# Optimization experiments

Measured on AMD Instinct MI355X. Metric: run time of the kernel, lower is better.

Reference implementation:

```python
import jax, jax.numpy as jnp
import numpy as np

B, N, DIM = 2, 2048, 1024
HEADS, DIM_HEAD, ROT = 16, 64, 32
SCALE = DIM_HEAD ** -0.5
INNER = HEADS * DIM_HEAD


def rotate_half(x):
    # '... (j d) -> ... j d' with j=2 -> split into first/second half
    d = x.shape[-1] // 2
    x1, x2 = x[..., :d], x[..., d:]
    return jnp.concatenate([-x2, x1], axis=-1)


def apply_rotary_pos_emb(freqs, t):
    rot = freqs.shape[-1]
    t1, t_pass = t[..., :rot], t[..., rot:]
    t1 = t1 * jnp.cos(freqs) + rotate_half(t1) * jnp.sin(freqs)
    return jnp.concatenate([t1, t_pass], axis=-1)


def setup_inputs() -> dict:
    key = jax.random.key(0)
    ks = jax.random.split(key, 5)
    x = jax.random.normal(ks[0], (B, N, DIM), dtype=jnp.float32)
    mask = jnp.ones((B, N), dtype=bool)
    rotary_pos_emb = jax.random.normal(ks[1], (N, ROT), dtype=jnp.float32)
    w_qkv = jax.random.normal(ks[2], (DIM, 3 * INNER), dtype=jnp.float32) * (DIM ** -0.5)
    w_out = jax.random.normal(ks[3], (INNER, DIM), dtype=jnp.float32) * (INNER ** -0.5)
    g = jnp.ones((DIM,), dtype=jnp.float32)
    return {"x": x, "mask": mask, "rotary_pos_emb": rotary_pos_emb,
            "w_qkv": w_qkv, "w_out": w_out, "g": g}


def reference(x, mask, rotary_pos_emb, w_qkv, w_out, g):
    b, n, _ = x.shape
    qkv = x @ w_qkv  # [b, n, 3*inner]
    q, k, v = jnp.split(qkv, 3, axis=-1)
    def to_heads(t):
        return t.reshape(b, n, HEADS, DIM_HEAD).transpose(0, 2, 1, 3)  # b h n d
    q, k, v = to_heads(q), to_heads(k), to_heads(v)
    q = q * SCALE
    # note: original applies rotary to q, k AND v
    q = apply_rotary_pos_emb(rotary_pos_emb, q)
    k = apply_rotary_pos_emb(rotary_pos_emb, k)
    v = apply_rotary_pos_emb(rotary_pos_emb, v)
    sim = jnp.einsum('bhid,bhjd->bhij', q, k)  # [b, h, n, n]
    neg = -jnp.finfo(sim.dtype).max
    sim = jnp.where(mask[:, None, None, :], sim, neg)
    causal_mask = jnp.triu(jnp.ones((n, n), dtype=bool), 1)
    sim = jnp.where(causal_mask, neg, sim)
    attn = jax.nn.softmax(sim.astype(jnp.float32), axis=-1).astype(sim.dtype)
    out = jnp.einsum('bhij,bhjd->bhid', attn, v)
    out = out.transpose(0, 2, 1, 3).reshape(b, n, INNER)
    out = out @ w_out
    # LayerNorm (no bias), eps=1e-5 for fp32, biased variance
    mean = jnp.mean(out, axis=-1, keepdims=True)
    var = jnp.var(out, axis=-1, keepdims=True)
    return (out - mean) * jax.lax.rsqrt(var + 1e-5) * g
```

## Files before the change

kernel.cpp:

```cpp
#include <hip/hip_runtime.h>
#include <stdint.h>

typedef unsigned short u16;
typedef __bf16 bf16x8 __attribute__((ext_vector_type(8)));
typedef float f32x4 __attribute__((ext_vector_type(4)));

#define B_ 2
#define N_ 2048
#define H_ 16
#define SCALE_ 0.125f
#define FM_ 11.0f

__device__ __forceinline__ float b2f(u16 u) {
    unsigned v = (unsigned)u << 16;
    float f;
    __builtin_memcpy(&f, &v, 4);
    return f;
}
__device__ __forceinline__ u16 f2b(float f) {
    unsigned x;
    __builtin_memcpy(&x, &f, 4);
    x = x + 0x7fff + ((x >> 16) & 1);
    return (u16)(x >> 16);
}

__global__ __launch_bounds__(256) void sentinel(float* __restrict__ out, int n, float val) {
    int i = blockIdx.x * 256 + threadIdx.x;
    if (i < n) out[i] = val;
}

__global__ __launch_bounds__(256) void conv_f2b(const float* __restrict__ in,
                                                u16* __restrict__ out, int n) {
    int i = (blockIdx.x * 256 + threadIdx.x) * 4;
    if (i >= n) return;
    float4 v = *(const float4*)(in + i);
    ushort4 o;
    o.x = f2b(v.x); o.y = f2b(v.y); o.z = f2b(v.z); o.w = f2b(v.w);
    *(ushort4*)(out + i) = o;
}

__global__ __launch_bounds__(256) void transpose_f2b(const float* __restrict__ in,
                                                     u16* __restrict__ out, int R, int C) {
    __shared__ float tile[32][33];
    int tx = threadIdx.x, ty = threadIdx.y;
    int c0 = blockIdx.x * 32, r0 = blockIdx.y * 32;
#pragma unroll
    for (int i = 0; i < 32; i += 8) tile[ty + i][tx] = in[(size_t)(r0 + ty + i) * C + c0 + tx];
    __syncthreads();
#pragma unroll
    for (int i = 0; i < 32; i += 8) out[(size_t)(c0 + ty + i) * R + r0 + tx] = f2b(tile[tx][ty + i]);
}

__global__ __launch_bounds__(256) void gemm_qkv(const u16* __restrict__ A, const u16* __restrict__ Bt,
                                                const float* __restrict__ freqs,
                                                u16* __restrict__ qo, u16* __restrict__ ko,
                                                u16* __restrict__ vt) {
    __shared__ __align__(16) u16 As[64 * 40];
    __shared__ __align__(16) u16 Bs[64 * 40];
    const int tid = threadIdx.x;
    const int wave = tid >> 6, lane = tid & 63;
    const int l15 = lane & 15, q4 = lane >> 4;
    const int m0 = blockIdx.y * 64, n0 = blockIdx.x * 64;
    const int srow = tid >> 2, scol = (tid & 3) * 8;
    f32x4 acc[4];
#pragma unroll
    for (int i = 0; i < 4; i++) acc[i] = (f32x4){0.f, 0.f, 0.f, 0.f};
    for (int k0 = 0; k0 < 1024; k0 += 32) {
        *(uint4*)&As[srow * 40 + scol] = *(const uint4*)&A[(size_t)(m0 + srow) * 1024 + k0 + scol];
        *(uint4*)&Bs[srow * 40 + scol] = *(const uint4*)&Bt[(size_t)(n0 + srow) * 1024 + k0 + scol];
        __syncthreads();
        bf16x8 a = *(const bf16x8*)&As[(wave * 16 + l15) * 40 + q4 * 8];
#pragma unroll
        for (int nt = 0; nt < 4; nt++) {
            bf16x8 b = *(const bf16x8*)&Bs[(nt * 16 + l15) * 40 + q4 * 8];
            acc[nt] = __builtin_amdgcn_mfma_f32_16x16x32_bf16(a, b, acc[nt], 0, 0, 0);
        }
        __syncthreads();
    }
    const int t = n0 >> 10;
    const int h = (n0 & 1023) >> 6;
#pragma unroll
    for (int r = 0; r < 4; r++) {
        int gm = m0 + wave * 16 + q4 * 4 + r;
        int b = gm >> 11, n = gm & 2047;
        float x0 = acc[0][r], x1 = acc[1][r], x2 = acc[2][r], x3 = acc[3][r];
        float f1 = freqs[n * 32 + l15];
        float f2 = freqs[n * 32 + 16 + l15];
        if (t == 0) { x0 *= SCALE_; x1 *= SCALE_; x2 *= SCALE_; x3 *= SCALE_; }
        float r0 = x0 * cosf(f1) - x1 * sinf(f1);
        float r1 = x1 * cosf(f2) + x0 * sinf(f2);
        int bh = b * H_ + h;
        if (t == 2) {
            u16* o = vt + (size_t)bh * 64 * N_;
            o[(l15) * N_ + n] = f2b(r0);
            o[(l15 + 16) * N_ + n] = f2b(r1);
            o[(l15 + 32) * N_ + n] = f2b(x2);
            o[(l15 + 48) * N_ + n] = f2b(x3);
        } else {
            u16* dst = (t == 0) ? qo : ko;
            u16* p = dst + ((size_t)bh * N_ + n) * 64;
            p[l15] = f2b(r0);
            p[l15 + 16] = f2b(r1);
            p[l15 + 32] = f2b(x2);
            p[l15 + 48] = f2b(x3);
        }
    }
}

__global__ __launch_bounds__(256) void attn(const u16* __restrict__ q, const u16* __restrict__ k,
                                            const u16* __restrict__ vt, u16* __restrict__ out) {
    __shared__ __align__(16) u16 Ks[2][64 * 72];
    __shared__ __align__(16) u16 Vs[2][64 * 72];
    __shared__ __align__(16) u16 Ps[64 * 72];
    const int tid = threadIdx.x, wave = tid >> 6, lane = tid & 63;
    const int l15 = lane & 15, q4 = lane >> 4;
    const int ta = blockIdx.x, tb = 31 - ta, bh = blockIdx.y;
    const u16* qp = q + (size_t)bh * N_ * 64;
    const u16* kp = k + (size_t)bh * N_ * 64;
    const u16* vp = vt + (size_t)bh * 64 * N_;
    const int b = bh >> 4, h = bh & 15;
    const int srow8 = tid >> 3, scol8 = (tid & 7) * 8;
    const int prow = (wave * 16 + l15) * 72;

    bf16x8 aqA0, aqA1, aqB0, aqB1;
    {
        int qr = ta * 64 + wave * 16;
        aqA0 = *(const bf16x8*)&qp[(qr + l15) * 64 + q4 * 8];
        aqA1 = *(const bf16x8*)&qp[(qr + l15) * 64 + 32 + q4 * 8];
        qr = tb * 64 + wave * 16;
        aqB0 = *(const bf16x8*)&qp[(qr + l15) * 64 + q4 * 8];
        aqB1 = *(const bf16x8*)&qp[(qr + l15) * 64 + 32 + q4 * 8];
    }
    f32x4 o[4];
#pragma unroll
    for (int i = 0; i < 4; i++) o[i] = (f32x4){0.f, 0.f, 0.f, 0.f};
    float psum = 0.f;

    auto stage = [&](int jt, int buf) {
#pragma unroll
        for (int i = 0; i < 64; i += 32) {
            *(uint4*)&Ks[buf][(i + srow8) * 72 + scol8] =
                *(const uint4*)&kp[(size_t)(jt * 64 + i + srow8) * 64 + scol8];
            *(uint4*)&Vs[buf][(i + srow8) * 72 + scol8] =
                *(const uint4*)&vp[(size_t)(i + srow8) * N_ + jt * 64 + scol8];
        }
    };
    auto iter = [&](bf16x8 aq0, bf16x8 aq1, int cur, int domask, int qa, int jb) {
#pragma unroll
        for (int kt = 0; kt < 4; kt++) {
            bf16x8 kf0 = *(const bf16x8*)&Ks[cur][(kt * 16 + l15) * 72 + q4 * 8];
            bf16x8 kf1 = *(const bf16x8*)&Ks[cur][(kt * 16 + l15) * 72 + 32 + q4 * 8];
            f32x4 z = (f32x4){0.f, 0.f, 0.f, 0.f};
            z = __builtin_amdgcn_mfma_f32_16x16x32_bf16(kf0, aq0, z, 0, 0, 0);
            z = __builtin_amdgcn_mfma_f32_16x16x32_bf16(kf1, aq1, z, 0, 0, 0);
            union { u16 u[4]; uint2 v; } pk;
            float ps = 0.f;
#pragma unroll
            for (int r = 0; r < 4; r++) {
                float s = z[r];
                if (domask) {
                    int key = jb * 64 + kt * 16 + q4 * 4 + r;
                    if (key > qa) s = -1e30f;
                }
                float p = __expf(s - FM_);
                ps += p;
                pk.u[r] = f2b(p);
            }
            psum += ps;
            *(uint2*)&Ps[prow + kt * 16 + q4 * 4] = pk.v;
        }
        bf16x8 pf0 = *(const bf16x8*)&Ps[prow + q4 * 8];
        bf16x8 pf1 = *(const bf16x8*)&Ps[prow + 32 + q4 * 8];
#pragma unroll
        for (int dt = 0; dt < 4; dt++) {
            bf16x8 v0 = *(const bf16x8*)&Vs[cur][(dt * 16 + l15) * 72 + q4 * 8];
            bf16x8 v1 = *(const bf16x8*)&Vs[cur][(dt * 16 + l15) * 72 + 32 + q4 * 8];
            o[dt] = __builtin_amdgcn_mfma_f32_16x16x32_bf16(v0, pf0, o[dt], 0, 0, 0);
            o[dt] = __builtin_amdgcn_mfma_f32_16x16x32_bf16(v1, pf1, o[dt], 0, 0, 0);
        }
    };
    auto epilogue = [&](int qt) {
        float v = psum;
        v += __shfl_xor(v, 16);
        v += __shfl_xor(v, 32);
        float inv = 1.f / v;
        int n = qt * 64 + wave * 16 + l15;
        u16* op = out + ((size_t)b * N_ + n) * 1024 + h * 64;
#pragma unroll
        for (int dt = 0; dt < 4; dt++) {
            union { u16 u[4]; uint2 v2; } w;
#pragma unroll
            for (int r = 0; r < 4; r++) w.u[r] = f2b(o[dt][r] * inv);
            *(uint2*)(op + dt * 16 + q4 * 4) = w.v2;
        }
#pragma unroll
        for (int i = 0; i < 4; i++) o[i] = (f32x4){0.f, 0.f, 0.f, 0.f};
        psum = 0.f;
    };

    stage(0, 0);
    int m = 0;
    for (int jb = 0; jb <= ta; jb++, m++) {
        int cur = m & 1;
        __syncthreads();
        stage((jb < ta) ? (jb + 1) : 0, cur ^ 1);
        iter(aqA0, aqA1, cur, jb == ta, ta * 64 + wave * 16 + l15, jb);
    }
    epilogue(ta);
    for (int jb = 0; jb <= tb; jb++, m++) {
        int cur = m & 1;
        __syncthreads();
        if (jb < tb) stage(jb + 1, cur ^ 1);
        iter(aqB0, aqB1, cur, jb == tb, tb * 64 + wave * 16 + l15, jb);
    }
    epilogue(tb);
}

__global__ __launch_bounds__(256) void gemm_out(const u16* __restrict__ A, const u16* __restrict__ Bt,
                                                float* __restrict__ C) {
    __shared__ __align__(16) u16 As[64 * 40];
    __shared__ __align__(16) u16 Bs[64 * 40];
    const int tid = threadIdx.x;
    const int wave = tid >> 6, lane = tid & 63;
    const int l15 = lane & 15, q4 = lane >> 4;
    const int m0 = blockIdx.y * 64, n0 = blockIdx.x * 64;
    const int srow = tid >> 2, scol = (tid & 3) * 8;
    f32x4 acc[4];
#pragma unroll
    for (int i = 0; i < 4; i++) acc[i] = (f32x4){0.f, 0.f, 0.f, 0.f};
    for (int k0 = 0; k0 < 1024; k0 += 32) {
        *(uint4*)&As[srow * 40 + scol] = *(const uint4*)&A[(size_t)(m0 + srow) * 1024 + k0 + scol];
        *(uint4*)&Bs[srow * 40 + scol] = *(const uint4*)&Bt[(size_t)(n0 + srow) * 1024 + k0 + scol];
        __syncthreads();
        bf16x8 a = *(const bf16x8*)&As[(wave * 16 + l15) * 40 + q4 * 8];
#pragma unroll
        for (int nt = 0; nt < 4; nt++) {
            bf16x8 b = *(const bf16x8*)&Bs[(nt * 16 + l15) * 40 + q4 * 8];
            acc[nt] = __builtin_amdgcn_mfma_f32_16x16x32_bf16(a, b, acc[nt], 0, 0, 0);
        }
        __syncthreads();
    }
#pragma unroll
    for (int nt = 0; nt < 4; nt++) {
#pragma unroll
        for (int r = 0; r < 4; r++) {
            int gm = m0 + wave * 16 + q4 * 4 + r;
            int gn = n0 + nt * 16 + l15;
            C[(size_t)gm * 1024 + gn] = acc[nt][r];
        }
    }
}

__global__ __launch_bounds__(256) void lnorm(const float* __restrict__ x, const float* __restrict__ g,
                                             float* __restrict__ out) {
    __shared__ float sh[8];
    int row = blockIdx.x, tid = threadIdx.x;
    float4 v = *(const float4*)(x + (size_t)row * 1024 + tid * 4);
    float s = v.x + v.y + v.z + v.w;
    float sq = v.x * v.x + v.y * v.y + v.z * v.z + v.w * v.w;
#pragma unroll
    for (int m = 1; m < 64; m <<= 1) {
        s += __shfl_xor(s, m);
        sq += __shfl_xor(sq, m);
    }
    if ((tid & 63) == 0) {
        sh[tid >> 6] = s;
        sh[4 + (tid >> 6)] = sq;
    }
    __syncthreads();
    s = sh[0] + sh[1] + sh[2] + sh[3];
    sq = sh[4] + sh[5] + sh[6] + sh[7];
    float mean = s * (1.f / 1024.f);
    float var = fmaxf(sq * (1.f / 1024.f) - mean * mean, 0.f);
    float rstd = rsqrtf(var + 1e-5f);
    float4 gv = *(const float4*)(g + tid * 4);
    float4 ov;
    ov.x = (v.x - mean) * rstd * gv.x;
    ov.y = (v.y - mean) * rstd * gv.y;
    ov.z = (v.z - mean) * rstd * gv.z;
    ov.w = (v.w - mean) * rstd * gv.w;
    *(float4*)(out + (size_t)row * 1024 + tid * 4) = ov;
}

extern "C" void kernel_launch(void* const* d_in, const int* in_sizes, int n_in,
                              void* d_out, int out_size, void* d_ws, size_t ws_size,
                              hipStream_t stream) {
    const float* x = nullptr;
    const float* rotf = nullptr;
    const float* wqkv = nullptr;
    const float* wout = nullptr;
    const float* g = nullptr;
    for (int i = 0; i < n_in; i++) {
        switch (in_sizes[i]) {
            case 4194304: x = (const float*)d_in[i]; break;
            case 65536:   rotf = (const float*)d_in[i]; break;
            case 3145728: wqkv = (const float*)d_in[i]; break;
            case 1048576: wout = (const float*)d_in[i]; break;
            case 1024:    g = (const float*)d_in[i]; break;
            default: break;
        }
    }
    int oblk = (out_size + 255) / 256;
    if (!(x && rotf && wqkv && wout && g)) {
        sentinel<<<oblk, 256, 0, stream>>>((float*)d_out, out_size, 200.f);
        return;
    }
    const size_t MB = 1024u * 1024;
    if (ws_size < 80 * MB) {
        sentinel<<<oblk, 256, 0, stream>>>((float*)d_out, out_size, 100.f);
        return;
    }
    char* ws = (char*)d_ws;
    u16* wqkvT = (u16*)(ws);
    u16* woutT = (u16*)(ws + 6 * MB);
    u16* xbf = (u16*)(ws + 8 * MB);
    u16* qbuf = (u16*)(ws + 16 * MB);
    u16* kbuf = (u16*)(ws + 24 * MB);
    u16* vtbuf = (u16*)(ws + 32 * MB);
    u16* abuf = (u16*)(ws + 40 * MB);
    float* pbuf = (float*)(ws + 48 * MB);

    conv_f2b<<<4096, 256, 0, stream>>>(x, xbf, 4194304);
    transpose_f2b<<<dim3(96, 32), dim3(32, 8), 0, stream>>>(wqkv, wqkvT, 1024, 3072);
    transpose_f2b<<<dim3(32, 32), dim3(32, 8), 0, stream>>>(wout, woutT, 1024, 1024);
    gemm_qkv<<<dim3(48, 64), 256, 0, stream>>>(xbf, wqkvT, rotf, qbuf, kbuf, vtbuf);
    attn<<<dim3(16, 32), 256, 0, stream>>>(qbuf, kbuf, vtbuf, abuf);
    gemm_out<<<dim3(16, 64), 256, 0, stream>>>(abuf, woutT, pbuf);
    lnorm<<<4096, 256, 0, stream>>>(pbuf, g, (float*)d_out);
}
```

Before: 240.0 us.

## Enlarge GEMM tiles to 128x128 and stage operands via direct global-to-LDS loads

Both projection GEMMs move from 64x64 block tiles, where each wave did a 16x64 slice, to 128x128 tiles where each wave computes a 64x64 sub-tile with 16 MFMA accumulators. This raises operand reuse from LDS and cuts global traffic per FLOP. Operands are now staged with global_load_lds 16-byte loads straight into unpadded LDS, skipping the register round trip. In exchange the kernels use more registers and launch fewer blocks, and the unpadded LDS layout may cause bank conflicts on fragment reads.

```diff
diff --git a/kernel.cpp b/kernel.cpp
--- a/kernel.cpp
+++ b/kernel.cpp
@@ -22,6 +22,12 @@
     __builtin_memcpy(&x, &f, 4);
     x = x + 0x7fff + ((x >> 16) & 1);
     return (u16)(x >> 16);
+}
+
+typedef const __attribute__((address_space(1))) unsigned int ga_uint;
+typedef __attribute__((address_space(3))) unsigned int ls_uint;
+__device__ __forceinline__ void gld_lds16(const void* g, void* l) {
+    __builtin_amdgcn_global_load_lds((ga_uint*)g, (ls_uint*)l, 16, 0, 0);
 }
 
 __global__ __launch_bounds__(256) void sentinel(float* __restrict__ out, int n, float val) {
@@ -55,54 +61,73 @@
                                                 const float* __restrict__ freqs,
                                                 u16* __restrict__ qo, u16* __restrict__ ko,
                                                 u16* __restrict__ vt) {
-    __shared__ __align__(16) u16 As[64 * 40];
-    __shared__ __align__(16) u16 Bs[64 * 40];
+    __shared__ __align__(16) u16 As[128 * 32];
+    __shared__ __align__(16) u16 Bs[128 * 32];
     const int tid = threadIdx.x;
     const int wave = tid >> 6, lane = tid & 63;
     const int l15 = lane & 15, q4 = lane >> 4;
-    const int m0 = blockIdx.y * 64, n0 = blockIdx.x * 64;
-    const int srow = tid >> 2, scol = (tid & 3) * 8;
-    f32x4 acc[4];
-#pragma unroll
-    for (int i = 0; i < 4; i++) acc[i] = (f32x4){0.f, 0.f, 0.f, 0.f};
+    const int m0 = blockIdx.y * 128, n0 = blockIdx.x * 128;
+    const int wm = (wave & 1) * 64, wn = (wave >> 1) * 64;
+    const int lrow = lane >> 2, lchunk = (lane & 3) * 8;
+    f32x4 acc[4][4];
+#pragma unroll
+    for (int i = 0; i < 4; i++)
+#pragma unroll
+        for (int j = 0; j < 4; j++) acc[i][j] = (f32x4){0.f, 0.f, 0.f, 0.f};
+
     for (int k0 = 0; k0 < 1024; k0 += 32) {
-        *(uint4*)&As[srow * 40 + scol] = *(const uint4*)&A[(size_t)(m0 + srow) * 1024 + k0 + scol];
-        *(uint4*)&Bs[srow * 40 + scol] = *(const uint4*)&Bt[(size_t)(n0 + srow) * 1024 + k0 + scol];
-        __syncthreads();
-        bf16x8 a = *(const bf16x8*)&As[(wave * 16 + l15) * 40 + q4 * 8];
-#pragma unroll
-        for (int nt = 0; nt < 4; nt++) {
-            bf16x8 b = *(const bf16x8*)&Bs[(nt * 16 + l15) * 40 + q4 * 8];
-            acc[nt] = __builtin_amdgcn_mfma_f32_16x16x32_bf16(a, b, acc[nt], 0, 0, 0);
-        }
-        __syncthreads();
-    }
-    const int t = n0 >> 10;
-    const int h = (n0 & 1023) >> 6;
-#pragma unroll
-    for (int r = 0; r < 4; r++) {
-        int gm = m0 + wave * 16 + q4 * 4 + r;
-        int b = gm >> 11, n = gm & 2047;
-        float x0 = acc[0][r], x1 = acc[1][r], x2 = acc[2][r], x3 = acc[3][r];
-        float f1 = freqs[n * 32 + l15];
-        float f2 = freqs[n * 32 + 16 + l15];
-        if (t == 0) { x0 *= SCALE_; x1 *= SCALE_; x2 *= SCALE_; x3 *= SCALE_; }
-        float r0 = x0 * cosf(f1) - x1 * sinf(f1);
-        float r1 = x1 * cosf(f2) + x0 * sinf(f2);
-        int bh = b * H_ + h;
-        if (t == 2) {
-            u16* o = vt + (size_t)bh * 64 * N_;
-            o[(l15) * N_ + n] = f2b(r0);
-            o[(l15 + 16) * N_ + n] = f2b(r1);
-            o[(l15 + 32) * N_ + n] = f2b(x2);
-            o[(l15 + 48) * N_ + n] = f2b(x3);
-        } else {
-            u16* dst = (t == 0) ? qo : ko;
-            u16* p = dst + ((size_t)bh * N_ + n) * 64;
-            p[l15] = f2b(r0);
-            p[l15 + 16] = f2b(r1);
-            p[l15 + 32] = f2b(x2);
-            p[l15 + 48] = f2b(x3);
+#pragma unroll
+        for (int i = 0; i < 2; i++) {
+            int row = wave * 32 + i * 16;
+            gld_lds16(&A[(size_t)(m0 + row + lrow) * 1024 + k0 + lchunk], &As[row * 32]);
+            gld_lds16(&Bt[(size_t)(n0 + row + lrow) * 1024 + k0 + lchunk], &Bs[row * 32]);
+        }
+        __syncthreads();
+        bf16x8 af[4], bf[4];
+#pragma unroll
+        for (int mt = 0; mt < 4; mt++)
+            af[mt] = *(const bf16x8*)&As[(wm + mt * 16 + l15) * 32 + q4 * 8];
+#pragma unroll
+        for (int nt = 0; nt < 4; nt++)
+            bf[nt] = *(const bf16x8*)&Bs[(wn + nt * 16 + l15) * 32 + q4 * 8];
+#pragma unroll
+        for (int mt = 0; mt < 4; mt++)
+#pragma unroll
+            for (int nt = 0; nt < 4; nt++)
+                acc[mt][nt] = __builtin_amdgcn_mfma_f32_16x16x32_bf16(af[mt], bf[nt], acc[mt][nt], 0, 0, 0);
+        __syncthreads();
+    }
+    const int qh = n0 + wn;
+    const int t = qh >> 10;
+    const int h = (qh & 1023) >> 6;
+#pragma unroll
+    for (int mt = 0; mt < 4; mt++) {
+#pragma unroll
+        for (int r = 0; r < 4; r++) {
+            int gm = m0 + wm + mt * 16 + q4 * 4 + r;
+            int b = gm >> 11, n = gm & 2047;
+            float x0 = acc[mt][0][r], x1 = acc[mt][1][r];
+            float x2 = acc[mt][2][r], x3 = acc[mt][3][r];
+            float f1 = freqs[n * 32 + l15];
+            float f2 = freqs[n * 32 + 16 + l15];
+            if (t == 0) { x0 *= SCALE_; x1 *= SCALE_; x2 *= SCALE_; x3 *= SCALE_; }
+            float r0 = x0 * cosf(f1) - x1 * sinf(f1);
+            float r1 = x1 * cosf(f2) + x0 * sinf(f2);
+            int bh = b * H_ + h;
+            if (t == 2) {
+                u16* o = vt + (size_t)bh * 64 * N_;
+                o[(l15) * N_ + n] = f2b(r0);
+                o[(l15 + 16) * N_ + n] = f2b(r1);
+                o[(l15 + 32) * N_ + n] = f2b(x2);
+                o[(l15 + 48) * N_ + n] = f2b(x3);
+            } else {
+                u16* dst = (t == 0) ? qo : ko;
+                u16* p = dst + ((size_t)bh * N_ + n) * 64;
+                p[l15] = f2b(r0);
+                p[l15 + 16] = f2b(r1);
+                p[l15 + 32] = f2b(x2);
+                p[l15 + 48] = f2b(x3);
+            }
         }
     }
 }
@@ -218,37 +243,52 @@
 
 __global__ __launch_bounds__(256) void gemm_out(const u16* __restrict__ A, const u16* __restrict__ Bt,
                                                 float* __restrict__ C) {
-    __shared__ __align__(16) u16 As[64 * 40];
-    __shared__ __align__(16) u16 Bs[64 * 40];
+    __shared__ __align__(16) u16 As[128 * 32];
+    __shared__ __align__(16) u16 Bs[128 * 32];
     const int tid = threadIdx.x;
     const int wave = tid >> 6, lane = tid & 63;
     const int l15 = lane & 15, q4 = lane >> 4;
-    const int m0 = blockIdx.y * 64, n0 = blockIdx.x * 64;
-    const int srow = tid >> 2, scol = (tid & 3) * 8;
-    f32x4 acc[4];
-#pragma unroll
-    for (int i = 0; i < 4; i++) acc[i] = (f32x4){0.f, 0.f, 0.f, 0.f};
+    const int m0 = blockIdx.y * 128, n0 = blockIdx.x * 128;
+    const int wm = (wave & 1) * 64, wn = (wave >> 1) * 64;
+    const int lrow = lane >> 2, lchunk = (lane & 3) * 8;
+    f32x4 acc[4][4];
+#pragma unroll
+    for (int i = 0; i < 4; i++)
+#pragma unroll
+        for (int j = 0; j < 4; j++) acc[i][j] = (f32x4){0.f, 0.f, 0.f, 0.f};
+
     for (int k0 = 0; k0 < 1024; k0 += 32) {
-        *(uint4*)&As[srow * 40 + scol] = *(const uint4*)&A[(size_t)(m0 + srow) * 1024 + k0 + scol];
-        *(uint4*)&Bs[srow * 40 + scol] = *(const uint4*)&Bt[(size_t)(n0 + srow) * 1024 + k0 + scol];
-        __syncthreads();
-        bf16x8 a = *(const bf16x8*)&As[(wave * 16 + l15) * 40 + q4 * 8];
-#pragma unroll
-        for (int nt = 0; nt < 4; nt++) {
-            bf16x8 b = *(const bf16x8*)&Bs[(nt * 16 + l15) * 40 + q4 * 8];
-            acc[nt] = __builtin_amdgcn_mfma_f32_16x16x32_bf16(a, b, acc[nt], 0, 0, 0);
-        }
-        __syncthreads();
-    }
-#pragma unroll
-    for (int nt = 0; nt < 4; nt++) {
-#pragma unroll
-        for (int r = 0; r < 4; r++) {
-            int gm = m0 + wave * 16 + q4 * 4 + r;
-            int gn = n0 + nt * 16 + l15;
-            C[(size_t)gm * 1024 + gn] = acc[nt][r];
-        }
-    }
+#pragma unroll
+        for (int i = 0; i < 2; i++) {
+            int row = wave * 32 + i * 16;
+            gld_lds16(&A[(size_t)(m0 + row + lrow) * 1024 + k0 + lchunk], &As[row * 32]);
+            gld_lds16(&Bt[(size_t)(n0 + row + lrow) * 1024 + k0 + lchunk], &Bs[row * 32]);
+        }
+        __syncthreads();
+        bf16x8 af[4], bf[4];
+#pragma unroll
+        for (int mt = 0; mt < 4; mt++)
+            af[mt] = *(const bf16x8*)&As[(wm + mt * 16 + l15) * 32 + q4 * 8];
+#pragma unroll
+        for (int nt = 0; nt < 4; nt++)
+            bf[nt] = *(const bf16x8*)&Bs[(wn + nt * 16 + l15) * 32 + q4 * 8];
+#pragma unroll
+        for (int mt = 0; mt < 4; mt++)
+#pragma unroll
+            for (int nt = 0; nt < 4; nt++)
+                acc[mt][nt] = __builtin_amdgcn_mfma_f32_16x16x32_bf16(af[mt], bf[nt], acc[mt][nt], 0, 0, 0);
+        __syncthreads();
+    }
+#pragma unroll
+    for (int mt = 0; mt < 4; mt++)
+#pragma unroll
+        for (int nt = 0; nt < 4; nt++)
+#pragma unroll
+            for (int r = 0; r < 4; r++) {
+                int gm = m0 + wm + mt * 16 + q4 * 4 + r;
+                int gn = n0 + wn + nt * 16 + l15;
+                C[(size_t)gm * 1024 + gn] = acc[mt][nt][r];
+            }
 }
 
 __global__ __launch_bounds__(256) void lnorm(const float* __restrict__ x, const float* __restrict__ g,
@@ -323,8 +363,8 @@
     conv_f2b<<<4096, 256, 0, stream>>>(x, xbf, 4194304);
     transpose_f2b<<<dim3(96, 32), dim3(32, 8), 0, stream>>>(wqkv, wqkvT, 1024, 3072);
     transpose_f2b<<<dim3(32, 32), dim3(32, 8), 0, stream>>>(wout, woutT, 1024, 1024);
-    gemm_qkv<<<dim3(48, 64), 256, 0, stream>>>(xbf, wqkvT, rotf, qbuf, kbuf, vtbuf);
+    gemm_qkv<<<dim3(24, 32), 256, 0, stream>>>(xbf, wqkvT, rotf, qbuf, kbuf, vtbuf);
     attn<<<dim3(16, 32), 256, 0, stream>>>(qbuf, kbuf, vtbuf, abuf);
-    gemm_out<<<dim3(16, 64), 256, 0, stream>>>(abuf, woutT, pbuf);
+    gemm_out<<<dim3(8, 32), 256, 0, stream>>>(abuf, woutT, pbuf);
     lnorm<<<4096, 256, 0, stream>>>(pbuf, g, (float*)d_out);
 }
```

Measured after the change: 413.7 us. 72.3% more time.
